# Performance work log

Measured on AMD Instinct MI355X. Metric: run time of the kernel, lower is better.

The kernel has to match this reference:

```python
import jax, jax.numpy as jnp
import numpy as np

B, SQ, SK, D, H = 4, 2048, 2048, 1024, 16
HD = D // H
SCALE = HD ** -0.5


def setup_inputs() -> dict:
    key = jax.random.key(0)
    ks = jax.random.split(key, 11)
    s = 0.02
    return {
        "query": jax.random.normal(ks[0], (B, SQ, D), jnp.float32),
        "key": jax.random.normal(ks[1], (B, SK, D), jnp.float32),
        "value": jax.random.normal(ks[2], (B, SK, D), jnp.float32),
        "Wq": jax.random.normal(ks[3], (D, D), jnp.float32) * s,
        "bq": jnp.zeros((D,), jnp.float32),
        "Wk": jax.random.normal(ks[4], (D, D), jnp.float32) * s,
        "bk": jnp.zeros((D,), jnp.float32),
        "Wv": jax.random.normal(ks[5], (D, D), jnp.float32) * s,
        "bv": jnp.zeros((D,), jnp.float32),
        "Wo": jax.random.normal(ks[6], (D, D), jnp.float32) * s,
        "bo": jnp.zeros((D,), jnp.float32),
    }


def reference(query, key, value, Wq, bq, Wk, bk, Wv, bv, Wo, bo):
    # Linear projections (torch nn.Linear: x @ W.T + b)
    Q = query @ Wq.T + bq          # (B, SQ, D)
    K = key @ Wk.T + bk            # (B, SK, D)
    V = value @ Wv.T + bv          # (B, SK, D)
    # split heads -> (B, H, S, HD)
    Q = Q.reshape(B, SQ, H, HD).transpose(0, 2, 1, 3)
    K = K.reshape(B, SK, H, HD).transpose(0, 2, 1, 3)
    V = V.reshape(B, SK, H, HD).transpose(0, 2, 1, 3)
    scores = jnp.einsum('bhqd,bhkd->bhqk', Q, K) * SCALE
    attn = jax.nn.softmax(scores, axis=-1)     # (B, H, SQ, SK); dropout=0 (eval)
    attended = jnp.einsum('bhqk,bhkd->bhqd', attn, V)
    attended = attended.mean(axis=1)           # head-average -> (B, SQ, HD)
    attended = jnp.tile(attended, (1, 1, H))   # repeat to (B, SQ, D)
    output = attended @ Wo.T + bo
    avg_attention = attn.mean(axis=1)          # (B, SQ, SK)
    return (output, avg_attention)
```

## Files before the change

### kernel.cpp

```cpp
#include <hip/hip_runtime.h>
#include <hip/hip_bf16.h>
#include <math.h>

#define BB 4
#define SQL 2048
#define SKL 2048
#define DM 1024
#define NH 16
#define HDIM 64
#define NSPLIT 2
#define QSCALE 0.18033688011112042f

typedef __attribute__((ext_vector_type(8))) short bf16x8;
typedef __attribute__((ext_vector_type(4))) float f32x4;
typedef __attribute__((ext_vector_type(16))) float f32x16;

__device__ __forceinline__ float exp2fast(float x) { return __builtin_amdgcn_exp2f(x); }
__device__ __forceinline__ float log2fast(float x) { return __builtin_amdgcn_logf(x); }

__device__ __forceinline__ unsigned short f2bf(float f) {
    union { __hip_bfloat16 h; unsigned short u; } c;
    c.h = __float2bfloat16(f);
    return c.u;
}

__device__ __forceinline__ unsigned cvtpk(float lo, float hi) {
    unsigned r;
    asm("v_cvt_pk_bf16_f32 %0, %1, %2" : "=v"(r) : "v"(lo), "v"(hi));
    return r;
}

__device__ __forceinline__ bf16x8 cvt8(const float4& a, const float4& b) {
    bf16x8 r;
    r[0] = (short)f2bf(a.x); r[1] = (short)f2bf(a.y);
    r[2] = (short)f2bf(a.z); r[3] = (short)f2bf(a.w);
    r[4] = (short)f2bf(b.x); r[5] = (short)f2bf(b.y);
    r[6] = (short)f2bf(b.z); r[7] = (short)f2bf(b.w);
    return r;
}

__device__ __forceinline__ void gload16(const void* g, void* l) {
    __builtin_amdgcn_global_load_lds(
        (const __attribute__((address_space(1))) unsigned int*)g,
        (__attribute__((address_space(3))) unsigned int*)l, 16, 0, 0);
}

#define VMCNT0() asm volatile("s_waitcnt vmcnt(0)" ::: "memory")

__global__ __launch_bounds__(256)
void wo_eff_kernel(const float* __restrict__ Wo, float* __restrict__ We) {
    int i = blockIdx.x * 256 + threadIdx.x;
    if (i < DM * HDIM) {
        int n = i >> 6, d = i & 63;
        float s = 0.f;
#pragma unroll
        for (int h = 0; h < NH; ++h) s += Wo[(size_t)n * DM + h * HDIM + d];
        We[i] = s;
    }
}

__global__ __launch_bounds__(256)
void proj_bf16(const float* __restrict__ X, const float* __restrict__ W,
               const float* __restrict__ bias, unsigned short* __restrict__ Y,
               float scale)
{
    __shared__ __align__(16) unsigned short As[128 * 32];
    __shared__ __align__(16) unsigned short Bs[128 * 32];
    const int tid = threadIdx.x;
    const int lane = tid & 63, wid = tid >> 6;
    const int g = lane >> 4, lm = lane & 15;
    const int wr = wid >> 1, wc = wid & 1;
    const int m0 = blockIdx.x * 128, n0 = blockIdx.y * 128;

    int rA[2], cA[2], offA[2];
#pragma unroll
    for (int i = 0; i < 2; ++i) {
        int q = tid + i * 256;
        rA[i] = q >> 2; cA[i] = q & 3;
        offA[i] = rA[i] * 32 + ((cA[i] ^ (rA[i] & 3)) << 3);
    }
    float4 xa[2][2], wa[2][2], xb[2][2], wb[2][2];
#pragma unroll
    for (int i = 0; i < 2; ++i) {
        const float* xp = &X[(size_t)(m0 + rA[i]) * DM + cA[i] * 8];
        const float* wp = &W[(size_t)(n0 + rA[i]) * DM + cA[i] * 8];
        xa[i][0] = *(const float4*)xp; xa[i][1] = *(const float4*)(xp + 4);
        wa[i][0] = *(const float4*)wp; wa[i][1] = *(const float4*)(wp + 4);
    }
    const f32x4 fz = {0.f, 0.f, 0.f, 0.f};
    f32x4 acc[4][4];
#pragma unroll
    for (int i = 0; i < 4; ++i)
#pragma unroll
        for (int j = 0; j < 4; ++j) acc[i][j] = fz;

    for (int t = 0; t < 32; ++t) {
        __syncthreads();
#pragma unroll
        for (int i = 0; i < 2; ++i) {
            *(bf16x8*)&As[offA[i]] = cvt8(xa[i][0], xa[i][1]);
            *(bf16x8*)&Bs[offA[i]] = cvt8(wa[i][0], wa[i][1]);
        }
        if (t < 31) {
            int k0 = (t + 1) * 32;
#pragma unroll
            for (int i = 0; i < 2; ++i) {
                const float* xp = &X[(size_t)(m0 + rA[i]) * DM + k0 + cA[i] * 8];
                const float* wp = &W[(size_t)(n0 + rA[i]) * DM + k0 + cA[i] * 8];
                xb[i][0] = *(const float4*)xp; xb[i][1] = *(const float4*)(xp + 4);
                wb[i][0] = *(const float4*)wp; wb[i][1] = *(const float4*)(wp + 4);
            }
        }
        __syncthreads();
        bf16x8 a[4], b[4];
#pragma unroll
        for (int f = 0; f < 4; ++f) {
            int ra = wr * 64 + f * 16 + lm;
            a[f] = *(const bf16x8*)&As[ra * 32 + (((g) ^ (ra & 3)) << 3)];
            int rb = wc * 64 + f * 16 + lm;
            b[f] = *(const bf16x8*)&Bs[rb * 32 + (((g) ^ (rb & 3)) << 3)];
        }
#pragma unroll
        for (int fm = 0; fm < 4; ++fm)
#pragma unroll
            for (int fn = 0; fn < 4; ++fn)
                acc[fm][fn] = __builtin_amdgcn_mfma_f32_16x16x32_bf16(
                    a[fm], b[fn], acc[fm][fn], 0, 0, 0);
        if (t < 31) {
#pragma unroll
            for (int i = 0; i < 2; ++i) {
                xa[i][0] = xb[i][0]; xa[i][1] = xb[i][1];
                wa[i][0] = wb[i][0]; wa[i][1] = wb[i][1];
            }
        }
    }
    float bn[4];
#pragma unroll
    for (int fn = 0; fn < 4; ++fn) bn[fn] = bias[n0 + wc * 64 + fn * 16 + lm];
#pragma unroll
    for (int fm = 0; fm < 4; ++fm)
#pragma unroll
        for (int i = 0; i < 4; ++i) {
            int m = m0 + wr * 64 + fm * 16 + 4 * g + i;
#pragma unroll
            for (int fn = 0; fn < 4; ++fn) {
                int n = n0 + wc * 64 + fn * 16 + lm;
                Y[(size_t)m * DM + n] = f2bf((acc[fm][fn][i] + bn[fn]) * scale);
            }
        }
}

__global__ __launch_bounds__(256)
void transpose_v(const unsigned short* __restrict__ V, unsigned short* __restrict__ Vt)
{
    __shared__ __align__(16) unsigned short Ts[64][80];
    const int tid = threadIdx.x;
    const int kv0 = blockIdx.x * 64, h = blockIdx.y, b = blockIdx.z;
#pragma unroll
    for (int i = 0; i < 2; ++i) {
        int q = tid + i * 256;
        int r = q >> 3, c = q & 7;
        *(uint4*)&Ts[r][c * 8] =
            *(const uint4*)&V[(size_t)(b * SKL + kv0 + r) * DM + h * HDIM + c * 8];
    }
    __syncthreads();
#pragma unroll
    for (int i = 0; i < 2; ++i) {
        int q = tid + i * 256;
        int d = q >> 3, kc = q & 7;
        union { unsigned short u16[8]; uint4 v; } tw;
#pragma unroll
        for (int e = 0; e < 8; ++e) tw.u16[e] = Ts[kc * 8 + e][d];
        *(uint4*)&Vt[((size_t)(b * NH + h) * HDIM + d) * SKL + kv0 + kc * 8] = tw.v;
    }
}

__global__ __launch_bounds__(256, 2)
void flash_mfma2(const unsigned short* __restrict__ Q,
                 const unsigned short* __restrict__ K,
                 const unsigned short* __restrict__ Vt,
                 float* __restrict__ lpart, float* __restrict__ Opart)
{
    __shared__ __align__(16) unsigned short sK[2][64 * 64];
    __shared__ __align__(16) unsigned short sV[2][64 * 64];
    const int tid = threadIdx.x;
    const int lane = tid & 63, wid = tid >> 6;
    const int l31 = lane & 31, h8 = lane >> 5;
    const int split = blockIdx.x & (NSPLIT - 1);
    const int q0 = (blockIdx.x >> 1) * 256;
    const int h = blockIdx.y, b = blockIdx.z;
    const int myq0 = q0 + wid * 32 + l31;
    const int myq1 = myq0 + 128;
    const int NT = SKL / 64 / NSPLIT;
    const int kt0 = split * NT;

    bf16x8 qf0[4], qf1[4];
    {
        const unsigned short* qp0 = &Q[(size_t)(b * SQL + myq0) * DM + h * HDIM + h8 * 8];
        const unsigned short* qp1 = &Q[(size_t)(b * SQL + myq1) * DM + h * HDIM + h8 * 8];
#pragma unroll
        for (int c = 0; c < 4; ++c) {
            qf0[c] = *(const bf16x8*)(qp0 + c * 16);
            qf1[c] = *(const bf16x8*)(qp1 + c * 16);
        }
    }

    int rr[2], cc[2];
#pragma unroll
    for (int i = 0; i < 2; ++i) {
        int s = tid + i * 256;
        rr[i] = s >> 3;
        cc[i] = ((s & 7) ^ (rr[i] & 7)) * 8;
    }
    const unsigned short* Kbase = &K[((size_t)b * SKL + kt0 * 64) * DM + h * HDIM];
    const unsigned short* Vbase = &Vt[((size_t)(b * NH + h) * HDIM) * SKL + kt0 * 64];

#pragma unroll
    for (int i = 0; i < 2; ++i) {
        gload16(Kbase + (size_t)rr[i] * DM + cc[i], &sK[0][(wid * 64 + i * 256) * 8]);
        gload16(Vbase + (size_t)rr[i] * SKL + cc[i], &sV[0][(wid * 64 + i * 256) * 8]);
    }
    VMCNT0();
    __syncthreads();

    const f32x16 z16 = {0.f};
    f32x16 o00 = z16, o01 = z16, o10 = z16, o11 = z16;
    float l0 = 0.f, l1 = 0.f;
    int cur = 0;

    for (int kt = 0; kt < NT; ++kt) {
        if (kt + 1 < NT) {
            int k0 = (kt + 1) * 64;
#pragma unroll
            for (int i = 0; i < 2; ++i) {
                gload16(Kbase + (size_t)(k0 + rr[i]) * DM + cc[i],
                        &sK[cur ^ 1][(wid * 64 + i * 256) * 8]);
                gload16(Vbase + (size_t)rr[i] * SKL + k0 + cc[i],
                        &sV[cur ^ 1][(wid * 64 + i * 256) * 8]);
            }
        }
        f32x16 c00 = z16, c01 = z16, c10 = z16, c11 = z16;
        __builtin_amdgcn_s_setprio(1);
#pragma unroll
        for (int c = 0; c < 4; ++c) {
            int cg = 2 * c + h8;
            bf16x8 a0 = *(const bf16x8*)&sK[cur][l31 * 64 + ((cg ^ (l31 & 7)) << 3)];
            bf16x8 a1 = *(const bf16x8*)&sK[cur][(32 + l31) * 64 + ((cg ^ (l31 & 7)) << 3)];
            c00 = __builtin_amdgcn_mfma_f32_32x32x16_bf16(a0, qf0[c], c00, 0, 0, 0);
            c01 = __builtin_amdgcn_mfma_f32_32x32x16_bf16(a1, qf0[c], c01, 0, 0, 0);
            c10 = __builtin_amdgcn_mfma_f32_32x32x16_bf16(a0, qf1[c], c10, 0, 0, 0);
            c11 = __builtin_amdgcn_mfma_f32_32x32x16_bf16(a1, qf1[c], c11, 0, 0, 0);
        }
        __builtin_amdgcn_s_setprio(0);
        bf16x8 ap0[4], ap1[4];
        {
            float ps = 0.f;
#pragma unroll
            for (int r = 0; r < 16; ++r) { c00[r] = exp2fast(c00[r]); ps += c00[r]; }
#pragma unroll
            for (int r = 0; r < 16; ++r) { c01[r] = exp2fast(c01[r]); ps += c01[r]; }
            ps += __shfl_xor(ps, 32);
            l0 += ps;
#pragma unroll
            for (int ks = 0; ks < 4; ++ks) {
                const int base = (ks & 1) * 8;
                const f32x16& ct = (ks & 2) ? c01 : c00;
                unsigned wA0 = cvtpk(ct[base + 0], ct[base + 1]);
                unsigned wA1 = cvtpk(ct[base + 2], ct[base + 3]);
                unsigned wB0 = cvtpk(ct[base + 4], ct[base + 5]);
                unsigned wB1 = cvtpk(ct[base + 6], ct[base + 7]);
                asm volatile("v_permlane32_swap_b32 %0, %1" : "+v"(wA0), "+v"(wB0));
                asm volatile("v_permlane32_swap_b32 %0, %1" : "+v"(wA1), "+v"(wB1));
                union { unsigned u[4]; bf16x8 v; } pu;
                pu.u[0] = wA0; pu.u[1] = wA1; pu.u[2] = wB0; pu.u[3] = wB1;
                ap0[ks] = pu.v;
            }
        }
        {
            float ps = 0.f;
#pragma unroll
            for (int r = 0; r < 16; ++r) { c10[r] = exp2fast(c10[r]); ps += c10[r]; }
#pragma unroll
            for (int r = 0; r < 16; ++r) { c11[r] = exp2fast(c11[r]); ps += c11[r]; }
            ps += __shfl_xor(ps, 32);
            l1 += ps;
#pragma unroll
            for (int ks = 0; ks < 4; ++ks) {
                const int base = (ks & 1) * 8;
                const f32x16& ct = (ks & 2) ? c11 : c10;
                unsigned wA0 = cvtpk(ct[base + 0], ct[base + 1]);
                unsigned wA1 = cvtpk(ct[base + 2], ct[base + 3]);
                unsigned wB0 = cvtpk(ct[base + 4], ct[base + 5]);
                unsigned wB1 = cvtpk(ct[base + 6], ct[base + 7]);
                asm volatile("v_permlane32_swap_b32 %0, %1" : "+v"(wA0), "+v"(wB0));
                asm volatile("v_permlane32_swap_b32 %0, %1" : "+v"(wA1), "+v"(wB1));
                union { unsigned u[4]; bf16x8 v; } pu;
                pu.u[0] = wA0; pu.u[1] = wA1; pu.u[2] = wB0; pu.u[3] = wB1;
                ap1[ks] = pu.v;
            }
        }
        __builtin_amdgcn_s_setprio(1);
#pragma unroll
        for (int ks = 0; ks < 4; ++ks) {
            int cg = 2 * ks + h8;
            bf16x8 v0 = *(const bf16x8*)&sV[cur][l31 * 64 + ((cg ^ (l31 & 7)) << 3)];
            bf16x8 v1 = *(const bf16x8*)&sV[cur][(32 + l31) * 64 + ((cg ^ (l31 & 7)) << 3)];
            o00 = __builtin_amdgcn_mfma_f32_32x32x16_bf16(v0, ap0[ks], o00, 0, 0, 0);
            o01 = __builtin_amdgcn_mfma_f32_32x32x16_bf16(v1, ap0[ks], o01, 0, 0, 0);
            o10 = __builtin_amdgcn_mfma_f32_32x32x16_bf16(v0, ap1[ks], o10, 0, 0, 0);
            o11 = __builtin_amdgcn_mfma_f32_32x32x16_bf16(v1, ap1[ks], o11, 0, 0, 0);
        }
        __builtin_amdgcn_s_setprio(0);
        VMCNT0();
        __syncthreads();
        cur ^= 1;
    }

    const size_t sb = (size_t)(split * BB + b);
    if (h8 == 0) {
        lpart[(sb * NH + h) * SQL + myq0] = l0;
        lpart[(sb * NH + h) * SQL + myq1] = l1;
    }
    float* Op0 = &Opart[((sb * NH + h) * SQL + myq0) * HDIM];
    float* Op1 = &Opart[((sb * NH + h) * SQL + myq1) * HDIM];
#pragma unroll
    for (int i2 = 0; i2 < 4; ++i2) {
        float4 w0, w1;
        int d = 8 * i2 + 4 * h8;
        w0.x = o00[4 * i2 + 0]; w0.y = o00[4 * i2 + 1];
        w0.z = o00[4 * i2 + 2]; w0.w = o00[4 * i2 + 3];
        w1.x = o01[4 * i2 + 0]; w1.y = o01[4 * i2 + 1];
        w1.z = o01[4 * i2 + 2]; w1.w = o01[4 * i2 + 3];
        *(float4*)(Op0 + d) = w0;
        *(float4*)(Op0 + d + 32) = w1;
        w0.x = o10[4 * i2 + 0]; w0.y = o10[4 * i2 + 1];
        w0.z = o10[4 * i2 + 2]; w0.w = o10[4 * i2 + 3];
        w1.x = o11[4 * i2 + 0]; w1.y = o11[4 * i2 + 1];
        w1.z = o11[4 * i2 + 2]; w1.w = o11[4 * i2 + 3];
        *(float4*)(Op1 + d) = w0;
        *(float4*)(Op1 + d + 32) = w1;
    }
}

__global__ __launch_bounds__(256)
void uw_combine(const float* __restrict__ lpart, float* __restrict__ uw,
                float* __restrict__ linv)
{
    int i = blockIdx.x * 256 + threadIdx.x;
    float l = lpart[i] + lpart[i + BB * NH * SQL];
    float ln = l * (float)NH;
    uw[i] = log2fast(ln);
    linv[i] = 1.0f / ln;
}

__global__ __launch_bounds__(256)
void am_reduce(const float* __restrict__ Opart, const float* __restrict__ linv,
               float* __restrict__ am)
{
    int i = blockIdx.x * 256 + threadIdx.x;
    int bq = i >> 4, c = i & 15;
    int b = bq >> 11, q = bq & 2047;
    const float* base = Opart + ((size_t)b * NH * SQL + q) * HDIM + c * 4;
    const float* il = linv + ((size_t)b * NH) * SQL + q;
    const size_t soff = (size_t)BB * NH * SQL * HDIM;
    float4 s = {0.f, 0.f, 0.f, 0.f};
    for (int h = 0; h < NH; ++h) {
        const float* p = base + (size_t)h * SQL * HDIM;
        float4 v0 = *(const float4*)p;
        float4 v1 = *(const float4*)(p + soff);
        float w = il[(size_t)h * SQL];
        s.x += (v0.x + v1.x) * w; s.y += (v0.y + v1.y) * w;
        s.z += (v0.z + v1.z) * w; s.w += (v0.w + v1.w) * w;
    }
    *(float4*)(am + (size_t)bq * HDIM + c * 4) = s;
}

__global__ __launch_bounds__(512)
void avg_mfma2(const unsigned short* __restrict__ Q, const unsigned short* __restrict__ K,
               const float* __restrict__ uw, float* __restrict__ avg)
{
    __shared__ __align__(16) unsigned short sQ[2][128 * 64];
    __shared__ __align__(16) unsigned short sK[2][128 * 64];
    __shared__ float uS[NH][128];
    const int tid = threadIdx.x;
    const int lane = tid & 63, wid = tid >> 6;
    const int g = lane >> 4, lm = lane & 15;
    const int wq = wid >> 1, wk = wid & 1;
    const int k0 = blockIdx.x * 128, q0 = blockIdx.y * 128, b = blockIdx.z;

    for (int i = tid; i < NH * 128; i += 512) {
        int hh = i >> 7, qq = i & 127;
        uS[hh][qq] = uw[(size_t)(b * NH + hh) * SQL + q0 + qq];
    }

    int rs[2], cs[2];
#pragma unroll
    for (int i = 0; i < 2; ++i) {
        int s = tid + i * 512;
        rs[i] = s >> 3;
        cs[i] = (s & 7) ^ (rs[i] & 7);
    }
    const unsigned short* Qbase = &Q[(size_t)(b * SQL + q0) * DM];
    const unsigned short* Kbase = &K[(size_t)(b * SKL + k0) * DM];
#pragma unroll
    for (int i = 0; i < 2; ++i) {
        gload16(Qbase + (size_t)rs[i] * DM + cs[i] * 8, &sQ[0][(tid + i * 512) * 8]);
        gload16(Kbase + (size_t)rs[i] * DM + cs[i] * 8, &sK[0][(tid + i * 512) * 8]);
    }
    VMCNT0();
    __syncthreads();

    const f32x4 fz = {0.f, 0.f, 0.f, 0.f};
    f32x4 acc[2][4];
#pragma unroll
    for (int mf = 0; mf < 2; ++mf)
#pragma unroll
        for (int nf = 0; nf < 4; ++nf) acc[mf][nf] = fz;

    int cur = 0;
    for (int hh = 0; hh < NH; ++hh) {
        if (hh + 1 < NH) {
#pragma unroll
            for (int i = 0; i < 2; ++i) {
                gload16(Qbase + (size_t)rs[i] * DM + (hh + 1) * HDIM + cs[i] * 8,
                        &sQ[cur ^ 1][(tid + i * 512) * 8]);
                gload16(Kbase + (size_t)rs[i] * DM + (hh + 1) * HDIM + cs[i] * 8,
                        &sK[cur ^ 1][(tid + i * 512) * 8]);
            }
        }
        f32x4 s[2][4];
#pragma unroll
        for (int mf = 0; mf < 2; ++mf)
#pragma unroll
            for (int nf = 0; nf < 4; ++nf) s[mf][nf] = fz;
        __builtin_amdgcn_s_setprio(1);
#pragma unroll
        for (int kk = 0; kk < 2; ++kk) {
            bf16x8 a[2];
#pragma unroll
            for (int mf = 0; mf < 2; ++mf) {
                int ra = wq * 32 + mf * 16 + lm;
                a[mf] = *(const bf16x8*)&sQ[cur][ra * 64 + (((kk * 4 + g) ^ (ra & 7)) << 3)];
            }
#pragma unroll
            for (int nf = 0; nf < 4; ++nf) {
                int rb = wk * 64 + nf * 16 + lm;
                bf16x8 kb = *(const bf16x8*)&sK[cur][rb * 64 + (((kk * 4 + g) ^ (rb & 7)) << 3)];
#pragma unroll
                for (int mf = 0; mf < 2; ++mf)
                    s[mf][nf] = __builtin_amdgcn_mfma_f32_16x16x32_bf16(
                        a[mf], kb, s[mf][nf], 0, 0, 0);
            }
        }
        __builtin_amdgcn_s_setprio(0);
#pragma unroll
        for (int mf = 0; mf < 2; ++mf)
#pragma unroll
            for (int i4 = 0; i4 < 4; ++i4) {
                float u = uS[hh][wq * 32 + mf * 16 + 4 * g + i4];
#pragma unroll
                for (int nf = 0; nf < 4; ++nf)
                    acc[mf][nf][i4] += exp2fast(s[mf][nf][i4] - u);
            }
        VMCNT0();
        __syncthreads();
        cur ^= 1;
    }
#pragma unroll
    for (int mf = 0; mf < 2; ++mf)
#pragma unroll
        for (int i4 = 0; i4 < 4; ++i4) {
            int qrow = q0 + wq * 32 + mf * 16 + 4 * g + i4;
#pragma unroll
            for (int nf = 0; nf < 4; ++nf)
                avg[(size_t)(b * SQL + qrow) * SKL + k0 + wk * 64 + nf * 16 + lm] =
                    acc[mf][nf][i4];
        }
}

__global__ __launch_bounds__(256)
void out_gemm(const float* __restrict__ amp, const float* __restrict__ We,
              const float* __restrict__ bo, float* __restrict__ out)
{
    __shared__ float As[64][68];
    __shared__ float Bs[64][68];
    const int m0 = blockIdx.x << 6, n0 = blockIdx.y << 6;
    const int tid = threadIdx.x;
    const int tx = tid & 15, ty = tid >> 4;
    const int lrow = tid >> 4, ldc = (tid & 15) << 2;
#pragma unroll
    for (int rr = 0; rr < 4; ++rr) {
        int r = (rr << 4) + lrow;
        float4 a = *reinterpret_cast<const float4*>(&amp[(size_t)(m0 + r) * HDIM + ldc]);
        float4 w = *reinterpret_cast<const float4*>(&We[(size_t)(n0 + r) * HDIM + ldc]);
        As[ldc + 0][r] = a.x; As[ldc + 1][r] = a.y; As[ldc + 2][r] = a.z; As[ldc + 3][r] = a.w;
        Bs[ldc + 0][r] = w.x; Bs[ldc + 1][r] = w.y; Bs[ldc + 2][r] = w.z; Bs[ldc + 3][r] = w.w;
    }
    __syncthreads();
    float acc[4][4] = {};
    for (int d = 0; d < 64; ++d) {
        float4 av = *reinterpret_cast<const float4*>(&As[d][ty << 2]);
        float4 bv = *reinterpret_cast<const float4*>(&Bs[d][tx << 2]);
        float aa[4] = {av.x, av.y, av.z, av.w};
        float bb[4] = {bv.x, bv.y, bv.z, bv.w};
#pragma unroll
        for (int i = 0; i < 4; ++i)
#pragma unroll
            for (int j = 0; j < 4; ++j)
                acc[i][j] = fmaf(aa[i], bb[j], acc[i][j]);
    }
    float4 bv = *reinterpret_cast<const float4*>(&bo[n0 + (tx << 2)]);
    float bb4[4] = {bv.x, bv.y, bv.z, bv.w};
#pragma unroll
    for (int i = 0; i < 4; ++i) {
        int m = m0 + (ty << 2) + i;
        float4 o = make_float4(acc[i][0] + bb4[0], acc[i][1] + bb4[1],
                               acc[i][2] + bb4[2], acc[i][3] + bb4[3]);
        *reinterpret_cast<float4*>(&out[(size_t)m * DM + n0 + (tx << 2)]) = o;
    }
}

extern "C" void kernel_launch(void* const* d_in, const int* in_sizes, int n_in,
                              void* d_out, int out_size, void* d_ws, size_t ws_size,
                              hipStream_t stream)
{
    const float* query = (const float*)d_in[0];
    const float* key   = (const float*)d_in[1];
    const float* value = (const float*)d_in[2];
    const float* Wq = (const float*)d_in[3];
    const float* bq = (const float*)d_in[4];
    const float* Wk = (const float*)d_in[5];
    const float* bk = (const float*)d_in[6];
    const float* Wv = (const float*)d_in[7];
    const float* bv = (const float*)d_in[8];
    const float* Wo = (const float*)d_in[9];
    const float* bo = (const float*)d_in[10];

    float* out0 = (float*)d_out;
    float* out_avg = out0 + (size_t)BB * SQL * DM;
    float* Opart = out_avg;

    const size_t nQ = (size_t)BB * SQL * DM;
    const size_t nML = (size_t)BB * NH * SQL;
    const size_t nAM = (size_t)BB * SQL * HDIM;
    unsigned short* Qb = (unsigned short*)d_ws;
    unsigned short* Kb = Qb + nQ;
    unsigned short* Vb = Kb + nQ;
    unsigned short* Vt = Vb + nQ;
    float* lpart = (float*)(Vt + nQ);
    float* uw   = lpart + NSPLIT * nML;
    float* linv = uw + nML;
    float* amb  = linv + nML;
    float* We   = amb + nAM;

    dim3 blk(256);
    wo_eff_kernel<<<dim3((DM * HDIM + 255) / 256), blk, 0, stream>>>(Wo, We);

    dim3 gp(64, 8);
    proj_bf16<<<gp, blk, 0, stream>>>(query, Wq, bq, Qb, QSCALE);
    proj_bf16<<<gp, blk, 0, stream>>>(key,   Wk, bk, Kb, 1.0f);
    proj_bf16<<<gp, blk, 0, stream>>>(value, Wv, bv, Vb, 1.0f);

    transpose_v<<<dim3(32, 16, 4), blk, 0, stream>>>(Vb, Vt);
    flash_mfma2<<<dim3(SQL / 256 * NSPLIT, NH, BB), blk, 0, stream>>>(Qb, Kb, Vt, lpart, Opart);
    uw_combine<<<dim3(512), blk, 0, stream>>>(lpart, uw, linv);
    am_reduce<<<dim3(512), blk, 0, stream>>>(Opart, linv, amb);
    avg_mfma2<<<dim3(SKL / 128, SQL / 128, BB), dim3(512), 0, stream>>>(Qb, Kb, uw, out_avg);
    out_gemm<<<dim3(128, 16), blk, 0, stream>>>(amb, We, bo, out0);
}
```

Baseline: 308.1 us.

## Widen flash blocks to 512 threads and read Q fragments directly in avg kernel

The flash attention kernel now runs 512 threads per block covering 512 query rows, so each K/V tile staged in shared memory serves twice as many queries and each thread issues one load per tile instead of two. The per-tile cross-half shuffle of the row sum moves out of the loop into a single reduction after it. In the attention-average kernel, the Q tile is no longer double-buffered in shared memory; each wave loads its Q fragments straight from global memory per head. This cuts LDS traffic and usage, but adds register pressure, reduces grid size and exposes global-load latency on Q.

```diff
diff --git a/kernel.cpp b/kernel.cpp
--- a/kernel.cpp
+++ b/kernel.cpp
@@ -175,7 +175,7 @@
     }
 }
 
-__global__ __launch_bounds__(256, 2)
+__global__ __launch_bounds__(512, 2)
 void flash_mfma2(const unsigned short* __restrict__ Q,
                  const unsigned short* __restrict__ K,
                  const unsigned short* __restrict__ Vt,
@@ -187,10 +187,10 @@
     const int lane = tid & 63, wid = tid >> 6;
     const int l31 = lane & 31, h8 = lane >> 5;
     const int split = blockIdx.x & (NSPLIT - 1);
-    const int q0 = (blockIdx.x >> 1) * 256;
+    const int q0 = (blockIdx.x >> 1) * 512;
     const int h = blockIdx.y, b = blockIdx.z;
     const int myq0 = q0 + wid * 32 + l31;
-    const int myq1 = myq0 + 128;
+    const int myq1 = myq0 + 256;
     const int NT = SKL / 64 / NSPLIT;
     const int kt0 = split * NT;
 
@@ -205,21 +205,13 @@
         }
     }
 
-    int rr[2], cc[2];
-#pragma unroll
-    for (int i = 0; i < 2; ++i) {
-        int s = tid + i * 256;
-        rr[i] = s >> 3;
-        cc[i] = ((s & 7) ^ (rr[i] & 7)) * 8;
-    }
+    const int rr = tid >> 3;
+    const int cc = ((tid & 7) ^ (rr & 7)) * 8;
     const unsigned short* Kbase = &K[((size_t)b * SKL + kt0 * 64) * DM + h * HDIM];
     const unsigned short* Vbase = &Vt[((size_t)(b * NH + h) * HDIM) * SKL + kt0 * 64];
 
-#pragma unroll
-    for (int i = 0; i < 2; ++i) {
-        gload16(Kbase + (size_t)rr[i] * DM + cc[i], &sK[0][(wid * 64 + i * 256) * 8]);
-        gload16(Vbase + (size_t)rr[i] * SKL + cc[i], &sV[0][(wid * 64 + i * 256) * 8]);
-    }
+    gload16(Kbase + (size_t)rr * DM + cc, &sK[0][tid * 8]);
+    gload16(Vbase + (size_t)rr * SKL + cc, &sV[0][tid * 8]);
     VMCNT0();
     __syncthreads();
 
@@ -231,13 +223,8 @@
     for (int kt = 0; kt < NT; ++kt) {
         if (kt + 1 < NT) {
             int k0 = (kt + 1) * 64;
-#pragma unroll
-            for (int i = 0; i < 2; ++i) {
-                gload16(Kbase + (size_t)(k0 + rr[i]) * DM + cc[i],
-                        &sK[cur ^ 1][(wid * 64 + i * 256) * 8]);
-                gload16(Vbase + (size_t)rr[i] * SKL + k0 + cc[i],
-                        &sV[cur ^ 1][(wid * 64 + i * 256) * 8]);
-            }
+            gload16(Kbase + (size_t)(k0 + rr) * DM + cc, &sK[cur ^ 1][tid * 8]);
+            gload16(Vbase + (size_t)rr * SKL + k0 + cc, &sV[cur ^ 1][tid * 8]);
         }
         f32x16 c00 = z16, c01 = z16, c10 = z16, c11 = z16;
         __builtin_amdgcn_s_setprio(1);
@@ -259,7 +246,6 @@
             for (int r = 0; r < 16; ++r) { c00[r] = exp2fast(c00[r]); ps += c00[r]; }
 #pragma unroll
             for (int r = 0; r < 16; ++r) { c01[r] = exp2fast(c01[r]); ps += c01[r]; }
-            ps += __shfl_xor(ps, 32);
             l0 += ps;
 #pragma unroll
             for (int ks = 0; ks < 4; ++ks) {
@@ -282,7 +268,6 @@
             for (int r = 0; r < 16; ++r) { c10[r] = exp2fast(c10[r]); ps += c10[r]; }
 #pragma unroll
             for (int r = 0; r < 16; ++r) { c11[r] = exp2fast(c11[r]); ps += c11[r]; }
-            ps += __shfl_xor(ps, 32);
             l1 += ps;
 #pragma unroll
             for (int ks = 0; ks < 4; ++ks) {
@@ -315,6 +300,9 @@
         __syncthreads();
         cur ^= 1;
     }
+
+    l0 += __shfl_xor(l0, 32);
+    l1 += __shfl_xor(l1, 32);
 
     const size_t sb = (size_t)(split * BB + b);
     if (h8 == 0) {
@@ -379,7 +367,6 @@
 void avg_mfma2(const unsigned short* __restrict__ Q, const unsigned short* __restrict__ K,
                const float* __restrict__ uw, float* __restrict__ avg)
 {
-    __shared__ __align__(16) unsigned short sQ[2][128 * 64];
     __shared__ __align__(16) unsigned short sK[2][128 * 64];
     __shared__ float uS[NH][128];
     const int tid = threadIdx.x;
@@ -403,10 +390,8 @@
     const unsigned short* Qbase = &Q[(size_t)(b * SQL + q0) * DM];
     const unsigned short* Kbase = &K[(size_t)(b * SKL + k0) * DM];
 #pragma unroll
-    for (int i = 0; i < 2; ++i) {
-        gload16(Qbase + (size_t)rs[i] * DM + cs[i] * 8, &sQ[0][(tid + i * 512) * 8]);
+    for (int i = 0; i < 2; ++i)
         gload16(Kbase + (size_t)rs[i] * DM + cs[i] * 8, &sK[0][(tid + i * 512) * 8]);
-    }
     VMCNT0();
     __syncthreads();
 
@@ -421,13 +406,17 @@
     for (int hh = 0; hh < NH; ++hh) {
         if (hh + 1 < NH) {
 #pragma unroll
-            for (int i = 0; i < 2; ++i) {
-                gload16(Qbase + (size_t)rs[i] * DM + (hh + 1) * HDIM + cs[i] * 8,
-                        &sQ[cur ^ 1][(tid + i * 512) * 8]);
+            for (int i = 0; i < 2; ++i)
                 gload16(Kbase + (size_t)rs[i] * DM + (hh + 1) * HDIM + cs[i] * 8,
                         &sK[cur ^ 1][(tid + i * 512) * 8]);
-            }
-        }
+        }
+        bf16x8 a[2][2];
+#pragma unroll
+        for (int kk = 0; kk < 2; ++kk)
+#pragma unroll
+            for (int mf = 0; mf < 2; ++mf)
+                a[kk][mf] = *(const bf16x8*)&Qbase[
+                    (size_t)(wq * 32 + mf * 16 + lm) * DM + hh * HDIM + (kk * 4 + g) * 8];
         f32x4 s[2][4];
 #pragma unroll
         for (int mf = 0; mf < 2; ++mf)
@@ -436,12 +425,6 @@
         __builtin_amdgcn_s_setprio(1);
 #pragma unroll
         for (int kk = 0; kk < 2; ++kk) {
-            bf16x8 a[2];
-#pragma unroll
-            for (int mf = 0; mf < 2; ++mf) {
-                int ra = wq * 32 + mf * 16 + lm;
-                a[mf] = *(const bf16x8*)&sQ[cur][ra * 64 + (((kk * 4 + g) ^ (ra & 7)) << 3)];
-            }
 #pragma unroll
             for (int nf = 0; nf < 4; ++nf) {
                 int rb = wk * 64 + nf * 16 + lm;
@@ -449,7 +432,7 @@
 #pragma unroll
                 for (int mf = 0; mf < 2; ++mf)
                     s[mf][nf] = __builtin_amdgcn_mfma_f32_16x16x32_bf16(
-                        a[mf], kb, s[mf][nf], 0, 0, 0);
+                        a[kk][mf], kb, s[mf][nf], 0, 0, 0);
             }
         }
         __builtin_amdgcn_s_setprio(0);
@@ -562,7 +545,8 @@
     proj_bf16<<<gp, blk, 0, stream>>>(value, Wv, bv, Vb, 1.0f);
 
     transpose_v<<<dim3(32, 16, 4), blk, 0, stream>>>(Vb, Vt);
-    flash_mfma2<<<dim3(SQL / 256 * NSPLIT, NH, BB), blk, 0, stream>>>(Qb, Kb, Vt, lpart, Opart);
+    flash_mfma2<<<dim3(SQL / 512 * NSPLIT, NH, BB), dim3(512), 0, stream>>>(
+        Qb, Kb, Vt, lpart, Opart);
     uw_combine<<<dim3(512), blk, 0, stream>>>(lpart, uw, linv);
     am_reduce<<<dim3(512), blk, 0, stream>>>(Opart, linv, amb);
     avg_mfma2<<<dim3(SKL / 128, SQL / 128, BB), dim3(512), 0, stream>>>(Qb, Kb, uw, out_avg);
```

New measurement: 330.5 us. 7.3% more time.
